# Performance work log

Hardware: AMD Instinct MI355X
Metric: run time of the kernel (lower is better)

The kernel has to match this reference:

```python
import jax, jax.numpy as jnp
import numpy as np

B, H, W = 16, 16, 16
L = 32          # in_capsules
O = 32          # out_capsules
P = 16          # p_size
PD = 4          # p_dim = sqrt(p_size)
ETA = 1.0


def setup_inputs() -> dict:
    key = jax.random.key(0)
    k1, k2, k3 = jax.random.split(key, 3)
    # [B, H, W, L*(P+1)]: first L*P channels are poses, last L are activations in [0,1]
    input_tensor = jax.random.uniform(k1, (B, H, W, L * (P + 1)), dtype=jnp.float32)
    # transform weights: [L, O, 4, 4] (kernel_size=1, shared over spatial positions)
    weights = jax.random.normal(k2, (L, O, PD, PD), dtype=jnp.float32) / np.sqrt(PD)
    activation_bias = jax.random.uniform(k3, (O,), dtype=jnp.float32)
    return {"input_tensor": input_tensor, "weights": weights,
            "activation_bias": activation_bias}


def reference(input_tensor, weights, activation_bias):
    Bs, Hh, Ww, _ = input_tensor.shape
    M = Hh * Ww
    # split poses / activations
    poses = input_tensor[..., : L * P].reshape(Bs, M, L, PD, PD)   # [B, M, L, 4, 4]
    acts = input_tensor[..., L * P:].reshape(Bs, M * L)            # [B, N]
    # votes[b, (m,l), o] = pose[b,m,l] @ W[l,o]  (shared transform, repeated over M)
    votes = jnp.einsum('bmlij,lojk->bmloik', poses, weights)
    votes = votes.reshape(Bs, M * L, O, P)                         # [B, N, O, 16]
    # weight votes by input activations and group per output capsule
    Y = (acts[:, :, None, None] * votes).transpose(0, 2, 1, 3)     # [B, O, N, 16]
    # top-1 right singular vector via gram matrix eigendecomposition (detached)
    gram = jnp.einsum('bonp,bonq->bopq', Y, Y)                     # [B, O, 16, 16]
    _, V = jnp.linalg.eigh(jax.lax.stop_gradient(gram))            # ascending eigvals
    pose_out = V[..., -1]                                          # [B, O, 16]
    # agreement: ||Y u||^2 / ||Y||_F^2
    yu = jnp.einsum('bonp,bop->bon', Y, pose_out)                  # [B, O, N]
    ratio = (yu ** 2).sum(-1) / (Y ** 2).sum((-1, -2))             # [B, O]
    act_out = jax.nn.sigmoid(ETA * (ratio - activation_bias))      # [B, O]
    return act_out, pose_out
```

## Files before the change

kernel.cpp:

```cpp
#include <hip/hip_runtime.h>

#define B_ 16
#define L_ 32
#define O_ 32
#define M_ 256
#define CH_ 544


__device__ __forceinline__ float rl(float v, int lane) {
  return __int_as_float(__builtin_amdgcn_readlane(__float_as_int(v), lane));
}

__device__ __forceinline__ float sum16_rl(float v) {
  float s = rl(v, 0);
#pragma unroll
  for (int j = 1; j < 16; j++) s += rl(v, j);
  return s;
}


__device__ __forceinline__ float slapy2f(float x, float y) {
  float xa = fabsf(x), ya = fabsf(y);
  float w = fmaxf(xa, ya), z = fminf(xa, ya);
  if (z == 0.f) return w;
  float q = z / w;
  return w * sqrtf(1.f + q * q);
}

__device__ __forceinline__ void slartgf(float f, float g, float* c, float* s, float* r) {
  if (g == 0.f) { *c = 1.f; *s = 0.f; *r = f; }
  else if (f == 0.f) { *c = 0.f; *s = copysignf(1.f, g); *r = fabsf(g); }
  else {
    float d = __builtin_amdgcn_sqrtf(f * f + g * g);
    float inv = __builtin_amdgcn_rcpf(d);
    *c = fabsf(f) * inv;
    *r = copysignf(d, f);
    *s = g * copysignf(inv, f);
  }
}

__device__ __forceinline__ void slaev2f(float a, float b, float c,
                                        float* rt1, float* rt2, float* cs1, float* sn1) {
  float sm = a + c, df = a - c;
  float adf = fabsf(df);
  float tb = b + b;
  float ab = fabsf(tb);
  float acmx, acmn;
  if (fabsf(a) > fabsf(c)) { acmx = a; acmn = c; } else { acmx = c; acmn = a; }
  float rt;
  if (adf > ab) { float q = ab / adf; rt = adf * sqrtf(1.f + q * q); }
  else if (adf < ab) { float q = adf / ab; rt = ab * sqrtf(1.f + q * q); }
  else rt = ab * sqrtf(2.f);
  int sgn1;
  if (sm < 0.f) { *rt1 = 0.5f * (sm - rt); sgn1 = -1; *rt2 = (acmx / *rt1) * acmn - (b / *rt1) * b; }
  else if (sm > 0.f) { *rt1 = 0.5f * (sm + rt); sgn1 = 1; *rt2 = (acmx / *rt1) * acmn - (b / *rt1) * b; }
  else { *rt1 = 0.5f * rt; *rt2 = -0.5f * rt; sgn1 = 1; }
  float cs; int sgn2;
  if (df >= 0.f) { cs = df + rt; sgn2 = 1; } else { cs = df - rt; sgn2 = -1; }
  float acs = fabsf(cs), c1, s1;
  if (acs > ab) { float ct = -tb / cs; s1 = 1.f / sqrtf(1.f + ct * ct); c1 = ct * s1; }
  else if (ab == 0.f) { c1 = 1.f; s1 = 0.f; }
  else { float tn = -cs / tb; c1 = 1.f / sqrtf(1.f + tn * tn); s1 = tn * c1; }
  if (sgn1 == sgn2) { float tn = c1; c1 = -s1; s1 = tn; }
  *cs1 = c1; *sn1 = s1;
}

__global__ __launch_bounds__(256) void moments_kernel(const float* __restrict__ in,
                                                      float* __restrict__ Tmom) {
  int bl = blockIdx.x;
  int b = bl >> 5, l = bl & 31;
  int t = threadIdx.x;
  int w = t >> 6, lane = t & 63;
  __shared__ __align__(16) float ut[4][16][68];
  const float* base = in + (size_t)b * (M_ * CH_);
  const float* row = base + (size_t)(w * 64 + lane) * CH_ + l * 16;
  float4 p0 = *(const float4*)(row + 0);
  float4 p1 = *(const float4*)(row + 4);
  float4 p2 = *(const float4*)(row + 8);
  float4 p3 = *(const float4*)(row + 12);
  float a = row[512 - l * 16 + l];
  float (*u)[68] = ut[w];
  u[0][lane] = a * p0.x;  u[1][lane] = a * p0.y;  u[2][lane] = a * p0.z;  u[3][lane] = a * p0.w;
  u[4][lane] = a * p1.x;  u[5][lane] = a * p1.y;  u[6][lane] = a * p1.z;  u[7][lane] = a * p1.w;
  u[8][lane] = a * p2.x;  u[9][lane] = a * p2.y;  u[10][lane] = a * p2.z; u[11][lane] = a * p2.w;
  u[12][lane] = a * p3.x; u[13][lane] = a * p3.y; u[14][lane] = a * p3.z; u[15][lane] = a * p3.w;
  asm volatile("" ::: "memory");
  int c = lane & 15, r0 = lane >> 4;
  float acc0 = 0.f, acc1 = 0.f, acc2 = 0.f, acc3 = 0.f;
#pragma unroll
  for (int m4 = 0; m4 < 64; m4 += 4) {
    float4 cv = *(const float4*)&u[c][m4];
    float4 a0 = *(const float4*)&u[r0][m4];
    float4 a1 = *(const float4*)&u[r0 + 4][m4];
    float4 a2 = *(const float4*)&u[r0 + 8][m4];
    float4 a3 = *(const float4*)&u[r0 + 12][m4];
    acc0 += a0.x * cv.x + a0.y * cv.y + a0.z * cv.z + a0.w * cv.w;
    acc1 += a1.x * cv.x + a1.y * cv.y + a1.z * cv.z + a1.w * cv.w;
    acc2 += a2.x * cv.x + a2.y * cv.y + a2.z * cv.z + a2.w * cv.w;
    acc3 += a3.x * cv.x + a3.y * cv.y + a3.z * cv.z + a3.w * cv.w;
  }
  float* dst = Tmom + ((size_t)bl * 4 + w) * 256;
  dst[r0 * 16 + c] = acc0;
  dst[(r0 + 4) * 16 + c] = acc1;
  dst[(r0 + 8) * 16 + c] = acc2;
  dst[(r0 + 12) * 16 + c] = acc3;
}

__global__ __launch_bounds__(64) void gram_eig_kernel(const float* __restrict__ Tmom,
                                                      const float* __restrict__ Wt,
                                                      const float* __restrict__ bias,
                                                      float* __restrict__ out) {
  int bo = blockIdx.x;
  int b = bo >> 5, o = bo & 31;
  int lane = threadIdx.x;

  __shared__ __align__(16) float4 Wall4[128];
  __shared__ __align__(16) float4 Tsh4[4 * 18];
  __shared__ float A[16][17];
  __shared__ __align__(16) float Zt[16][16];
  __shared__ float wvec[16];

  const float4* Wt4 = (const float4*)Wt;
#pragma unroll
  for (int k = 0; k < 2; k++) {
    int idx = lane + 64 * k;
    int l = idx >> 2, part = idx & 3;
    Wall4[idx] = Wt4[(l * 32 + o) * 4 + part];
  }
  __syncthreads();

  int p = lane >> 2;
  int i_ = p >> 2, k_ = p & 3;
  int i2 = lane & 3;
  float gx = 0.f, gy = 0.f, gz = 0.f, gw = 0.f;
  const float4* T4b = (const float4*)Tmom + (size_t)(b * 32) * 4 * 64;
  const float* WallF = (const float*)Wall4;
  float4 tc0 = T4b[0 * 64 + lane], tc1 = T4b[1 * 64 + lane];
  float4 tc2 = T4b[2 * 64 + lane], tc3 = T4b[3 * 64 + lane];
  float4 tn0 = T4b[4 * 64 + lane], tn1 = T4b[5 * 64 + lane];
  float4 tn2 = T4b[6 * 64 + lane], tn3 = T4b[7 * 64 + lane];
  for (int l = 0; l < 32; l++) {
    float4 tsum;
    tsum.x = (tc0.x + tc1.x) + (tc2.x + tc3.x);
    tsum.y = (tc0.y + tc1.y) + (tc2.y + tc3.y);
    tsum.z = (tc0.z + tc1.z) + (tc2.z + tc3.z);
    tsum.w = (tc0.w + tc1.w) + (tc2.w + tc3.w);
    __syncthreads();
    Tsh4[(lane >> 4) * 18 + (lane & 15)] = tsum;
    __syncthreads();
    tc0 = tn0; tc1 = tn1; tc2 = tn2; tc3 = tn3;
    if (l + 2 < 32) {
      const float4* nb = T4b + (size_t)(l + 2) * 4 * 64;
      tn0 = nb[0 * 64 + lane]; tn1 = nb[1 * 64 + lane];
      tn2 = nb[2 * 64 + lane]; tn3 = nb[3 * 64 + lane];
    }
    float4 wq0 = Wall4[l * 4 + 0], wq1 = Wall4[l * 4 + 1];
    float4 wq2 = Wall4[l * 4 + 2], wq3 = Wall4[l * 4 + 3];
#pragma unroll
    for (int jj = 0; jj < 4; jj++) {
      float4 trow = Tsh4[i_ * 18 + jj * 4 + i2];
      float ux = trow.x * wq0.x + trow.y * wq1.x + trow.z * wq2.x + trow.w * wq3.x;
      float uy = trow.x * wq0.y + trow.y * wq1.y + trow.z * wq2.y + trow.w * wq3.y;
      float uz = trow.x * wq0.z + trow.y * wq1.z + trow.z * wq2.z + trow.w * wq3.z;
      float uw = trow.x * wq0.w + trow.y * wq1.w + trow.z * wq2.w + trow.w * wq3.w;
      float wk = WallF[l * 16 + jj * 4 + k_];
      gx += wk * ux; gy += wk * uy; gz += wk * uz; gw += wk * uw;
    }
  }
  {
    int q0 = i2 * 4;
    A[p][q0 + 0] = gx; A[p][q0 + 1] = gy; A[p][q0 + 2] = gz; A[p][q0 + 3] = gw;
  }
  __syncthreads();
  float trace = sum16_rl((lane < 16) ? A[lane][lane] : 0.f);

  float dreg = 0.f, ereg = 0.f, taureg = 0.f;
  for (int i = 0; i < 15; i++) {
    float alpha = A[i + 1][i];
    float xv = (lane >= i + 2 && lane < 16) ? A[lane][i] : 0.f;
    float xn2 = sum16_rl(xv * xv);
    float taui;
    if (xn2 == 0.f) {
      taui = 0.f;
      if (lane == i) ereg = alpha;
    } else {
      float xnorm = sqrtf(xn2);
      float beta = -copysignf(slapy2f(alpha, xnorm), alpha);
      taui = (beta - alpha) / beta;
      float rs = 1.f / (alpha - beta);
      if (lane >= i + 2 && lane < 16) A[lane][i] = xv * rs;
      if (lane == i) ereg = beta;
      float wr = 0.f;
      if (lane >= i + 1 && lane < 16) {
        for (int cc = i + 1; cc < 16; cc++) {
          float av = (lane >= cc) ? A[lane][cc] : A[cc][lane];
          float vc = (cc == i + 1) ? 1.f : A[cc][i];
          wr += av * vc;
        }
        wr *= taui;
      }
      float vr = (lane == i + 1) ? 1.f : ((lane >= i + 2 && lane < 16) ? A[lane][i] : 0.f);
      float dot = sum16_rl(wr * vr);
      float alph2 = -0.5f * taui * dot;
      wr += alph2 * vr;
      if (lane < 16) wvec[lane] = wr;
      if (lane >= i + 1 && lane < 16) {
        float vl = vr;
        for (int cc = i + 1; cc <= lane; cc++) {
          float vc = (cc == i + 1) ? 1.f : A[cc][i];
          A[lane][cc] -= vl * wvec[cc] + wr * vc;
        }
      }
    }
    if (lane == i) { dreg = A[i][i]; taureg = taui; }
  }
  if (lane == 15) dreg = A[15][15];

  float z[16];
#pragma unroll
  for (int r = 0; r < 16; r++) z[r] = (lane == r) ? 1.f : 0.f;
  for (int i = 13; i >= 0; i--) {
    float taui = rl(taureg, i);
    if (taui != 0.f) {
      float s = 0.f;
#pragma unroll
      for (int r = 0; r < 16; r++) {
        float vr = (r == i + 1) ? 1.f : ((r >= i + 2) ? A[r][i] : 0.f);
        s += vr * z[r];
      }
      s *= taui;
#pragma unroll
      for (int r = 0; r < 16; r++) {
        float vr = (r == i + 1) ? 1.f : ((r >= i + 2) ? A[r][i] : 0.f);
        z[r] -= vr * s;
      }
    }
  }
  if (lane < 16) {
    float4* zt4 = (float4*)&Zt[lane][0];
    zt4[0] = make_float4(z[0], z[1], z[2], z[3]);
    zt4[1] = make_float4(z[4], z[5], z[6], z[7]);
    zt4[2] = make_float4(z[8], z[9], z[10], z[11]);
    zt4[3] = make_float4(z[12], z[13], z[14], z[15]);
  }
  __syncthreads();

  const float eps = 5.9604645e-08f;
  const float eps2 = eps * eps;
  const float safmin = 1.17549435e-38f;
  int l1 = 0, jtot = 0;
  const int nmaxit = 480;
  float dsh = __shfl(dreg, (lane + 1) & 63, 64);

  while (l1 < 16) {
    if (l1 > 0) { if (lane == l1 - 1) ereg = 0.f; }
    bool co = (lane < 15) &&
              ((ereg == 0.f) ||
               (fabsf(ereg) <= __builtin_amdgcn_sqrtf(fabsf(dreg)) *
                                   __builtin_amdgcn_sqrtf(fabsf(dsh)) * eps));
    unsigned long long bm = __ballot(co) & ~((1ull << l1) - 1ull);
    int m = bm ? (__ffsll(bm) - 1) : 15;
    if (m < 15) { if (lane == m) ereg = 0.f; }
    int l = l1, lend = m;
    l1 = m + 1;
    if (lend == l) continue;
    {
      float dl = rl(dreg, l), dle = rl(dreg, lend);
      if (fabsf(dle) < fabsf(dl)) { int tq = l; l = lend; lend = tq; }
    }

    if (lend > l) {
      for (;;) {
        bool cj = (lane < 15) && ((ereg * ereg) <= eps2 * fabsf(dreg) * fabsf(dsh) + safmin);
        int mq;
        if (l != lend) {
          unsigned long long bb2 = __ballot(cj) & ((1ull << lend) - 1ull) & ~((1ull << l) - 1ull);
          mq = bb2 ? (__ffsll(bb2) - 1) : lend;
        } else mq = lend;
        if (mq < lend) { if (lane == mq) ereg = 0.f; }
        if (mq == l) { l++; if (l <= lend) continue; break; }
        if (mq == l + 1) {
          float d_l = rl(dreg, l), e_l = rl(ereg, l), d_l1 = rl(dreg, l + 1);
          float rt1, rt2, cc, ss;
          slaev2f(d_l, e_l, d_l1, &rt1, &rt2, &cc, &ss);
          if (lane < 16) {
            float z1 = Zt[l + 1][lane], z0 = Zt[l][lane];
            Zt[l + 1][lane] = cc * z1 - ss * z0;
            Zt[l][lane] = ss * z1 + cc * z0;
          }
          if (lane == l) { dreg = rt1; ereg = 0.f; dsh = rt2; }
          if (lane == l + 1) dreg = rt2;
          if (lane == l - 1) dsh = rt1;
          l += 2; if (l <= lend) continue; break;
        }
        if (jtot == nmaxit) break;
        jtot++;
        float d0 = dreg, e0 = ereg;
        float pp = rl(d0, l);
        float e_lv = rl(e0, l);
        float gg = (rl(d0, l + 1) - pp) / (2.f * e_lv);
        float rr = slapy2f(gg, 1.f);
        gg = rl(d0, mq) - pp + e_lv / (gg + copysignf(rr, gg));
        float ss_ = 1.f, cc_ = 1.f;
        pp = 0.f;
        float zc = (lane < 16) ? Zt[mq][lane] : 0.f;
        for (int i = mq - 1; i >= l; i--) {
          float z0 = (lane < 16) ? Zt[i][lane] : 0.f;
          float e_i = rl(e0, i), d_i = rl(d0, i), d_i1 = rl(d0, i + 1);
          float ff = ss_ * e_i, bb = cc_ * e_i;
          slartgf(gg, ff, &cc_, &ss_, &rr);
          if (i != mq - 1) { if (lane == i + 1) ereg = rr; }
          gg = d_i1 - pp;
          rr = (d_i - gg) * ss_ + 2.f * cc_ * bb;
          pp = ss_ * rr;
          float dnew = gg + pp;
          if (lane == i + 1) dreg = dnew;
          if (lane == i) dsh = dnew;
          gg = cc_ * rr - bb;
          if (lane < 16) Zt[i + 1][lane] = cc_ * zc + ss_ * z0;
          zc = -ss_ * zc + cc_ * z0;
        }
        if (lane < 16) Zt[l][lane] = zc;
        float dlv = rl(d0, l) - pp;
        if (lane == l) { dreg = dlv; ereg = gg; }
        if (lane == l - 1) dsh = dlv;
      }
    } else {
      for (;;) {
        bool cj = (lane < 15) && ((ereg * ereg) <= eps2 * fabsf(dreg) * fabsf(dsh) + safmin);
        int mq;
        if (l != lend) {
          unsigned long long bb2 = __ballot(cj) & ((1ull << l) - 1ull) & ~((1ull << lend) - 1ull);
          mq = bb2 ? (63 - __clzll(bb2) + 1) : lend;
        } else mq = lend;
        if (mq > lend) { if (lane == mq - 1) ereg = 0.f; }
        if (mq == l) { l--; if (l >= lend) continue; break; }
        if (mq == l - 1) {
          float d_lm1 = rl(dreg, l - 1), e_lm1 = rl(ereg, l - 1), d_l = rl(dreg, l);
          float rt1, rt2, cc, ss;
          slaev2f(d_lm1, e_lm1, d_l, &rt1, &rt2, &cc, &ss);
          if (lane < 16) {
            float z1 = Zt[l][lane], z0 = Zt[l - 1][lane];
            Zt[l][lane] = cc * z1 - ss * z0;
            Zt[l - 1][lane] = ss * z1 + cc * z0;
          }
          if (lane == l - 1) { dreg = rt1; ereg = 0.f; dsh = rt2; }
          if (lane == l) dreg = rt2;
          if (lane == l - 2) dsh = rt1;
          l -= 2; if (l >= lend) continue; break;
        }
        if (jtot == nmaxit) break;
        jtot++;
        float d0 = dreg, e0 = ereg;
        float pp = rl(d0, l);
        float e_lm1 = rl(e0, l - 1);
        float gg = (rl(d0, l - 1) - pp) / (2.f * e_lm1);
        float rr = slapy2f(gg, 1.f);
        gg = rl(d0, mq) - pp + e_lm1 / (gg + copysignf(rr, gg));
        float ss_ = 1.f, cc_ = 1.f;
        pp = 0.f;
        float zc = (lane < 16) ? Zt[mq][lane] : 0.f;
        for (int i = mq; i <= l - 1; i++) {
          float z1 = (lane < 16) ? Zt[i + 1][lane] : 0.f;
          float e_i = rl(e0, i), d_i = rl(d0, i), d_i1 = rl(d0, i + 1);
          float ff = ss_ * e_i, bb = cc_ * e_i;
          slartgf(gg, ff, &cc_, &ss_, &rr);
          if (i != mq) { if (lane == i - 1) ereg = rr; }
          gg = d_i - pp;
          rr = (d_i1 - gg) * ss_ + 2.f * cc_ * bb;
          pp = ss_ * rr;
          float dnew = gg + pp;
          if (lane == i) dreg = dnew;
          if (lane == i - 1) dsh = dnew;
          gg = cc_ * rr - bb;
          if (lane < 16) Zt[i][lane] = ss_ * z1 + cc_ * zc;
          zc = cc_ * z1 - ss_ * zc;
        }
        if (lane < 16) Zt[l][lane] = zc;
        float dlv = rl(d0, l) - pp;
        if (lane == l) dreg = dlv;
        if (lane == l - 1) { ereg = gg; dsh = dlv; }
      }
    }
  }

  float mx = rl(dreg, 0);
  int k = 0;
#pragma unroll
  for (int j = 1; j < 16; j++) {
    float dj = rl(dreg, j);
    if (dj > mx) { mx = dj; k = j; }
  }
  float ratio = mx / trace;
  float act = 1.f / (1.f + expf(-(ratio - bias[o])));
  if (lane < 16) out[512 + bo * 16 + lane] = Zt[k][lane];
  if (lane == 0) out[bo] = act;
}

extern "C" void kernel_launch(void* const* d_in, const int* in_sizes, int n_in,
                              void* d_out, int out_size, void* d_ws, size_t ws_size,
                              hipStream_t stream) {
  const float* in = (const float*)d_in[0];
  const float* w = (const float*)d_in[1];
  const float* bias = (const float*)d_in[2];
  float* out = (float*)d_out;
  float* Tmom = (float*)d_ws;

  moments_kernel<<<B_ * L_, 256, 0, stream>>>(in, Tmom);
  gram_eig_kernel<<<B_ * O_, 64, 0, stream>>>(Tmom, w, bias, out);
}
```

Measured before the change: 152.3 us.

## Move Householder tridiagonalization into registers and drop block barriers

The tridiagonal reduction now keeps each column of the 16x16 Gram matrix in per-lane registers and exchanges Householder vectors with readlane instead of going through shared memory. It also stores the reflectors in registers for forming Q. With a single 64-lane wavefront per block, __syncthreads calls are replaced by compiler memory fences. Exact divisions and sqrt are swapped for hardware rcp/rsq approximations, and the next Zt row is prefetched in the QL/QR sweeps. The changes target serial LDS latency and barrier cost, but they add register pressure and slightly change floating-point accuracy.

```diff
diff --git a/kernel.cpp b/kernel.cpp
--- a/kernel.cpp
+++ b/kernel.cpp
@@ -18,12 +18,15 @@
   return s;
 }
 
+__device__ __forceinline__ float frcp(float x) { return __builtin_amdgcn_rcpf(x); }
+__device__ __forceinline__ float frsq(float x) { return __builtin_amdgcn_rsqf(x); }
+
 
 __device__ __forceinline__ float slapy2f(float x, float y) {
   float xa = fabsf(x), ya = fabsf(y);
   float w = fmaxf(xa, ya), z = fminf(xa, ya);
   if (z == 0.f) return w;
-  float q = z / w;
+  float q = z * frcp(w);
   return w * sqrtf(1.f + q * q);
 }
 
@@ -31,8 +34,9 @@
   if (g == 0.f) { *c = 1.f; *s = 0.f; *r = f; }
   else if (f == 0.f) { *c = 0.f; *s = copysignf(1.f, g); *r = fabsf(g); }
   else {
-    float d = __builtin_amdgcn_sqrtf(f * f + g * g);
-    float inv = __builtin_amdgcn_rcpf(d);
+    float t = f * f + g * g;
+    float inv = frsq(t);
+    float d = t * inv;
     *c = fabsf(f) * inv;
     *r = copysignf(d, f);
     *s = g * copysignf(inv, f);
@@ -118,7 +122,6 @@
   __shared__ __align__(16) float4 Tsh4[4 * 18];
   __shared__ float A[16][17];
   __shared__ __align__(16) float Zt[16][16];
-  __shared__ float wvec[16];
 
   const float4* Wt4 = (const float4*)Wt;
 #pragma unroll
@@ -127,7 +130,7 @@
     int l = idx >> 2, part = idx & 3;
     Wall4[idx] = Wt4[(l * 32 + o) * 4 + part];
   }
-  __syncthreads();
+  asm volatile("" ::: "memory");
 
   int p = lane >> 2;
   int i_ = p >> 2, k_ = p & 3;
@@ -145,9 +148,8 @@
     tsum.y = (tc0.y + tc1.y) + (tc2.y + tc3.y);
     tsum.z = (tc0.z + tc1.z) + (tc2.z + tc3.z);
     tsum.w = (tc0.w + tc1.w) + (tc2.w + tc3.w);
-    __syncthreads();
     Tsh4[(lane >> 4) * 18 + (lane & 15)] = tsum;
-    __syncthreads();
+    asm volatile("" ::: "memory");
     tc0 = tn0; tc1 = tn1; tc2 = tn2; tc3 = tn3;
     if (l + 2 < 32) {
       const float4* nb = T4b + (size_t)(l + 2) * 4 * 64;
@@ -166,74 +168,88 @@
       float wk = WallF[l * 16 + jj * 4 + k_];
       gx += wk * ux; gy += wk * uy; gz += wk * uz; gw += wk * uw;
     }
+    asm volatile("" ::: "memory");
   }
   {
     int q0 = i2 * 4;
     A[p][q0 + 0] = gx; A[p][q0 + 1] = gy; A[p][q0 + 2] = gz; A[p][q0 + 3] = gw;
   }
-  __syncthreads();
-  float trace = sum16_rl((lane < 16) ? A[lane][lane] : 0.f);
+  asm volatile("" ::: "memory");
+
+  int c16 = lane & 15;
+  float a[16];
+#pragma unroll
+  for (int r = 0; r < 16; r++) a[r] = A[r][c16];
+
+  float trace;
+  {
+    float diag = 0.f;
+#pragma unroll
+    for (int r = 0; r < 16; r++) if (c16 == r) diag = a[r];
+    trace = sum16_rl((lane < 16) ? diag : 0.f);
+  }
 
   float dreg = 0.f, ereg = 0.f, taureg = 0.f;
+  float hv[14];
+#pragma unroll
   for (int i = 0; i < 15; i++) {
-    float alpha = A[i + 1][i];
-    float xv = (lane >= i + 2 && lane < 16) ? A[lane][i] : 0.f;
-    float xn2 = sum16_rl(xv * xv);
-    float taui;
+    float cn = 0.f;
+#pragma unroll
+    for (int r = i + 2; r < 16; r++) cn += a[r] * a[r];
+    float xn2 = rl(cn, i);
+    float alpha = rl(a[i + 1], i);
+    float taui = 0.f;
+    float vc = 0.f;
     if (xn2 == 0.f) {
-      taui = 0.f;
       if (lane == i) ereg = alpha;
     } else {
       float xnorm = sqrtf(xn2);
       float beta = -copysignf(slapy2f(alpha, xnorm), alpha);
       taui = (beta - alpha) / beta;
       float rs = 1.f / (alpha - beta);
-      if (lane >= i + 2 && lane < 16) A[lane][i] = xv * rs;
       if (lane == i) ereg = beta;
-      float wr = 0.f;
-      if (lane >= i + 1 && lane < 16) {
-        for (int cc = i + 1; cc < 16; cc++) {
-          float av = (lane >= cc) ? A[lane][cc] : A[cc][lane];
-          float vc = (cc == i + 1) ? 1.f : A[cc][i];
-          wr += av * vc;
-        }
-        wr *= taui;
-      }
-      float vr = (lane == i + 1) ? 1.f : ((lane >= i + 2 && lane < 16) ? A[lane][i] : 0.f);
-      float dot = sum16_rl(wr * vr);
+      vc = (lane == i + 1) ? 1.f : ((lane >= i + 2 && lane < 16) ? a[i] * rs : 0.f);
+      float vb[16];
+#pragma unroll
+      for (int r = i + 1; r < 16; r++) vb[r] = rl(vc, r);
+      float acc = 0.f;
+#pragma unroll
+      for (int r = i + 1; r < 16; r++) acc += a[r] * vb[r];
+      float wc = (lane >= i + 1 && lane < 16) ? taui * acc : 0.f;
+      float wb[16];
+#pragma unroll
+      for (int r = i + 1; r < 16; r++) wb[r] = rl(wc, r);
+      float dot = 0.f;
+#pragma unroll
+      for (int r = i + 1; r < 16; r++) dot += vb[r] * wb[r];
       float alph2 = -0.5f * taui * dot;
-      wr += alph2 * vr;
-      if (lane < 16) wvec[lane] = wr;
-      if (lane >= i + 1 && lane < 16) {
-        float vl = vr;
-        for (int cc = i + 1; cc <= lane; cc++) {
-          float vc = (cc == i + 1) ? 1.f : A[cc][i];
-          A[lane][cc] -= vl * wvec[cc] + wr * vc;
-        }
-      }
-    }
-    if (lane == i) { dreg = A[i][i]; taureg = taui; }
-  }
-  if (lane == 15) dreg = A[15][15];
+      wc += alph2 * vc;
+#pragma unroll
+      for (int r = i + 1; r < 16; r++) wb[r] += alph2 * vb[r];
+#pragma unroll
+      for (int r = i + 1; r < 16; r++) a[r] -= vb[r] * wc + wb[r] * vc;
+    }
+    if (i < 14) hv[i] = vc;
+    if (lane == i) taureg = taui;
+  }
+#pragma unroll
+  for (int r = 0; r < 16; r++) if (c16 == r) dreg = a[r];
+  if (lane >= 16) dreg = 0.f;
 
   float z[16];
 #pragma unroll
   for (int r = 0; r < 16; r++) z[r] = (lane == r) ? 1.f : 0.f;
+#pragma unroll
   for (int i = 13; i >= 0; i--) {
     float taui = rl(taureg, i);
     if (taui != 0.f) {
+      float vbq[16];
       float s = 0.f;
 #pragma unroll
-      for (int r = 0; r < 16; r++) {
-        float vr = (r == i + 1) ? 1.f : ((r >= i + 2) ? A[r][i] : 0.f);
-        s += vr * z[r];
-      }
+      for (int r = i + 1; r < 16; r++) { vbq[r] = rl(hv[i], r); s += vbq[r] * z[r]; }
       s *= taui;
 #pragma unroll
-      for (int r = 0; r < 16; r++) {
-        float vr = (r == i + 1) ? 1.f : ((r >= i + 2) ? A[r][i] : 0.f);
-        z[r] -= vr * s;
-      }
+      for (int r = i + 1; r < 16; r++) z[r] -= vbq[r] * s;
     }
   }
   if (lane < 16) {
@@ -243,7 +259,7 @@
     zt4[2] = make_float4(z[8], z[9], z[10], z[11]);
     zt4[3] = make_float4(z[12], z[13], z[14], z[15]);
   }
-  __syncthreads();
+  asm volatile("" ::: "memory");
 
   const float eps = 5.9604645e-08f;
   const float eps2 = eps * eps;
@@ -298,14 +314,16 @@
         float d0 = dreg, e0 = ereg;
         float pp = rl(d0, l);
         float e_lv = rl(e0, l);
-        float gg = (rl(d0, l + 1) - pp) / (2.f * e_lv);
+        float gg = (rl(d0, l + 1) - pp) * 0.5f * frcp(e_lv);
         float rr = slapy2f(gg, 1.f);
-        gg = rl(d0, mq) - pp + e_lv / (gg + copysignf(rr, gg));
+        gg = rl(d0, mq) - pp + e_lv * frcp(gg + copysignf(rr, gg));
         float ss_ = 1.f, cc_ = 1.f;
         pp = 0.f;
         float zc = (lane < 16) ? Zt[mq][lane] : 0.f;
+        float znxt = (lane < 16) ? Zt[mq - 1][lane] : 0.f;
         for (int i = mq - 1; i >= l; i--) {
-          float z0 = (lane < 16) ? Zt[i][lane] : 0.f;
+          float z0 = znxt;
+          if (i > l) znxt = (lane < 16) ? Zt[i - 1][lane] : 0.f;
           float e_i = rl(e0, i), d_i = rl(d0, i), d_i1 = rl(d0, i + 1);
           float ff = ss_ * e_i, bb = cc_ * e_i;
           slartgf(gg, ff, &cc_, &ss_, &rr);
@@ -354,14 +372,16 @@
         float d0 = dreg, e0 = ereg;
         float pp = rl(d0, l);
         float e_lm1 = rl(e0, l - 1);
-        float gg = (rl(d0, l - 1) - pp) / (2.f * e_lm1);
+        float gg = (rl(d0, l - 1) - pp) * 0.5f * frcp(e_lm1);
         float rr = slapy2f(gg, 1.f);
-        gg = rl(d0, mq) - pp + e_lm1 / (gg + copysignf(rr, gg));
+        gg = rl(d0, mq) - pp + e_lm1 * frcp(gg + copysignf(rr, gg));
         float ss_ = 1.f, cc_ = 1.f;
         pp = 0.f;
         float zc = (lane < 16) ? Zt[mq][lane] : 0.f;
+        float znxt = (lane < 16) ? Zt[mq + 1][lane] : 0.f;
         for (int i = mq; i <= l - 1; i++) {
-          float z1 = (lane < 16) ? Zt[i + 1][lane] : 0.f;
+          float z1 = znxt;
+          if (i < l - 1) znxt = (lane < 16) ? Zt[i + 2][lane] : 0.f;
           float e_i = rl(e0, i), d_i = rl(d0, i), d_i1 = rl(d0, i + 1);
           float ff = ss_ * e_i, bb = cc_ * e_i;
           slartgf(gg, ff, &cc_, &ss_, &rr);
@@ -383,6 +403,7 @@
       }
     }
   }
+  asm volatile("" ::: "memory");
 
   float mx = rl(dreg, 0);
   int k = 0;
```

Measured after the change: 132.6 us. -12.9%, faster.
